# Performance work log

Measured on AMD Instinct MI355X. Metric: run time of the kernel, lower is better.

## Reference

```python
import jax, jax.numpy as jnp
import numpy as np

SEP = 64  # separate_number


def _get_histogram(M, sep):
    # torch code detaches + moves to CPU: no gradient flows through the histogram
    M = jax.lax.stop_gradient(M)
    mn = jnp.min(M)
    mx = jnp.max(M)
    interval = (mx - mn) / sep
    # equal-width binning; last bin is inclusive of max (clip handles it)
    idx = jnp.clip(jnp.floor((M - mn) / interval).astype(jnp.int32), 0, sep - 1)
    hist = jnp.zeros((sep,), dtype=M.dtype).at[idx.ravel()].add(1.0)
    return jax.nn.sigmoid(hist)


def setup_inputs() -> dict:
    key = jax.random.key(0)
    k1, k2, k3 = jax.random.split(key, 3)
    N, D = 8192, 256
    current_feature = jax.random.normal(k1, (N, D), dtype=jnp.float32)
    previous_feature = jax.random.normal(k2, (N, D), dtype=jnp.float32)
    # nn.Linear(separate_number, hidden_dim=1, bias=False) weight: [1, SEP]
    W = jax.random.normal(k3, (1, SEP), dtype=jnp.float32) * (1.0 / np.sqrt(SEP))
    return {"current_feature": current_feature, "previous_feature": previous_feature, "W": W}


def reference(current_feature, previous_feature, W):
    sep = W.shape[1]
    # [N, N] similarity matrix
    M = jnp.matmul(current_feature, previous_feature.T)
    hist_left = _get_histogram(M, sep)
    # result_matrix_right = prev @ cur.T = M.T; a transpose has an identical
    # value histogram, so reuse M (same math, avoids a second NxN matmul)
    hist_right = _get_histogram(M, sep)
    beta = (hist_left + hist_right) / 2.0
    beta = jnp.matmul(beta, W.T)  # Linear, no bias -> [hidden_dim]
    return jax.nn.sigmoid(beta)
```

## Files before the change

kernel.cpp:

```cpp
#include <hip/hip_runtime.h>

typedef __attribute__((ext_vector_type(8))) short short8v;
typedef __attribute__((ext_vector_type(4))) float f32x4;

#define N_ROWS 8192
#define KSPLIT 768
#define SEP 64
#define TDET 65.0f
#define TEXACT 73.0f
#define VTOL 5.5f
#define LIST_CAP 524288u

__device__ inline unsigned f2ord(float x){
  unsigned u = __float_as_uint(x);
  return (u & 0x80000000u) ? ~u : (u | 0x80000000u);
}
__device__ inline float ord2f(unsigned u){
  unsigned b = (u & 0x80000000u) ? (u & 0x7fffffffu) : ~u;
  return __uint_as_float(b);
}
__device__ inline unsigned short bf16rn(float x){
  unsigned b = __float_as_uint(x);
  unsigned r = (b + 0x7fffu + ((b >> 16) & 1u)) >> 16;
  return (unsigned short)r;
}
__device__ inline void gload16(const void* g, void* l){
  __builtin_amdgcn_global_load_lds((const __attribute__((address_space(1))) void*)g,
                                   (__attribute__((address_space(3))) void*)l, 16, 0, 0);
}
__device__ inline int bin_of(float v, float mnv, float interval){
  float r = (v - mnv) / interval;
  int b = (int)floorf(r);
  return b < 0 ? 0 : (b > 63 ? 63 : b);
}

__global__ void split_kernel(const float* __restrict__ cur, const float* __restrict__ prev,
                             unsigned short* __restrict__ cur2, unsigned short* __restrict__ prev2,
                             unsigned* __restrict__ ctl){
  if (blockIdx.x == 0){
    if (threadIdx.x == 0){
      ctl[0] = 0xFFFFFFFFu; ctl[1] = 0u; ctl[2] = 1u; ctl[3] = 0u; ctl[4] = 0u; ctl[5] = 0u;
    }
    if (threadIdx.x < 64) ctl[6 + threadIdx.x] = 0u;
  }
  int g = blockIdx.x * blockDim.x + threadIdx.x;
  int isB = (g >= (N_ROWS * 256 / 4)) ? 1 : 0;
  int t = g - isB * (N_ROWS * 256 / 4);
  const float4 v = ((const float4*)(isB ? prev : cur))[t];
  int row = t >> 6;
  int col = (t & 63) << 2;
  float xs[4] = {v.x, v.y, v.z, v.w};
  unsigned short h[4], l[4];
  #pragma unroll
  for (int j = 0; j < 4; ++j){
    unsigned short hb = bf16rn(xs[j]);
    float hf = __uint_as_float(((unsigned)hb) << 16);
    h[j] = hb;
    l[j] = bf16rn(xs[j] - hf);
  }
  unsigned short* dst = isB ? prev2 : cur2;
  size_t base = (size_t)row * KSPLIT + col;
  uint2 hw, lw;
  hw.x = (unsigned)h[0] | ((unsigned)h[1] << 16); hw.y = (unsigned)h[2] | ((unsigned)h[3] << 16);
  lw.x = (unsigned)l[0] | ((unsigned)l[1] << 16); lw.y = (unsigned)l[2] | ((unsigned)l[3] << 16);
  *(uint2*)(dst + base) = hw;
  if (!isB){
    *(uint2*)(dst + base + 256) = lw;
    *(uint2*)(dst + base + 512) = hw;
  } else {
    *(uint2*)(dst + base + 256) = hw;
    *(uint2*)(dst + base + 512) = lw;
  }
}

template<int EPI, int KSTEPS>
__global__ __launch_bounds__(256) void gemm_kernel(const unsigned short* __restrict__ A2,
                                                   const unsigned short* __restrict__ B2,
                                                   unsigned* __restrict__ mm,
                                                   unsigned* __restrict__ hist,
                                                   unsigned* __restrict__ idxq,
                                                   unsigned* __restrict__ lcnt,
                                                   const unsigned* __restrict__ flag){
  if (EPI == 0 || EPI == 2){
    if (flag[0] == 0u) return;
  }
  __shared__ unsigned short As[128 * 32];
  __shared__ unsigned short Bs[128 * 32];

  const int tid  = threadIdx.x;
  const int lane = tid & 63;
  const int wave = tid >> 6;
  const int swz = ((blockIdx.x & 7) << 9) | (blockIdx.x >> 3);
  const int bm = swz >> 6;
  const int bn = swz & 63;
  const int wr = wave >> 1, wc = wave & 1;

  const size_t aBase = (size_t)bm * 128 * KSPLIT;
  const size_t bBase = (size_t)bn * 128 * KSPLIT;
  const int id0 = tid, id1 = tid + 256;
  const size_t aOff0 = aBase + (size_t)(id0 >> 2) * KSPLIT + (id0 & 3) * 8;
  const size_t aOff1 = aBase + (size_t)(id1 >> 2) * KSPLIT + (id1 & 3) * 8;
  const size_t bOff0 = bBase + (size_t)(id0 >> 2) * KSPLIT + (id0 & 3) * 8;
  const size_t bOff1 = bBase + (size_t)(id1 >> 2) * KSPLIT + (id1 & 3) * 8;

  f32x4 acc[4][4];
  #pragma unroll
  for (int m = 0; m < 4; ++m)
    #pragma unroll
    for (int n = 0; n < 4; ++n)
      acc[m][n] = (f32x4){0.f, 0.f, 0.f, 0.f};

  const int rsel = lane & 15;
  const int ksel = (lane >> 4) * 8;

  for (int ks = 0; ks < KSTEPS; ++ks){
    const int k0 = ks * 32;
    gload16(A2 + aOff0 + k0, As + id0 * 8);
    gload16(A2 + aOff1 + k0, As + id1 * 8);
    gload16(B2 + bOff0 + k0, Bs + id0 * 8);
    gload16(B2 + bOff1 + k0, Bs + id1 * 8);
    __syncthreads();
    short8v a[4], b[4];
    #pragma unroll
    for (int m = 0; m < 4; ++m)
      a[m] = *(const short8v*)(As + (wr * 64 + m * 16 + rsel) * 32 + ksel);
    #pragma unroll
    for (int n = 0; n < 4; ++n)
      b[n] = *(const short8v*)(Bs + (wc * 64 + n * 16 + rsel) * 32 + ksel);
    #pragma unroll
    for (int m = 0; m < 4; ++m)
      #pragma unroll
      for (int n = 0; n < 4; ++n)
        acc[m][n] = __builtin_amdgcn_mfma_f32_16x16x32_bf16(a[m], b[n], acc[m][n], 0, 0, 0);
    __syncthreads();
  }

  float*    red = (float*)As;
  unsigned* lh  = (unsigned*)((char*)As + 64);

  if (EPI == 0){
    float mn = 3.4e38f, mx = -3.4e38f;
    #pragma unroll
    for (int m = 0; m < 4; ++m)
      #pragma unroll
      for (int n = 0; n < 4; ++n)
        #pragma unroll
        for (int q = 0; q < 4; ++q){
          float v = acc[m][n][q];
          mn = fminf(mn, v); mx = fmaxf(mx, v);
        }
    #pragma unroll
    for (int off = 32; off; off >>= 1){
      mn = fminf(mn, __shfl_xor(mn, off));
      mx = fmaxf(mx, __shfl_xor(mx, off));
    }
    if (lane == 0){ red[wave] = mn; red[4 + wave] = mx; }
    __syncthreads();
    if (tid == 0){
      mn = fminf(fminf(red[0], red[1]), fminf(red[2], red[3]));
      mx = fmaxf(fmaxf(red[4], red[5]), fmaxf(red[6], red[7]));
      atomicMin(mm + 0, f2ord(mn));
      atomicMax(mm + 1, f2ord(mx));
    }
  }
  if (EPI == 2){
    if (tid < SEP) lh[tid] = 0u;
    __syncthreads();
    const float mnv = ord2f(mm[0]);
    const float mxv = ord2f(mm[1]);
    const float interval = (mxv - mnv) / 64.0f;
    #pragma unroll
    for (int m = 0; m < 4; ++m)
      #pragma unroll
      for (int n = 0; n < 4; ++n)
        #pragma unroll
        for (int q = 0; q < 4; ++q)
          atomicAdd(&lh[bin_of(acc[m][n][q], mnv, interval)], 1u);
    __syncthreads();
    if (tid < SEP){ unsigned c = lh[tid]; if (c) atomicAdd(hist + tid, c); }
  }
  if (EPI == 4){
    unsigned long long mask = 0ull;
    #pragma unroll
    for (int m = 0; m < 4; ++m)
      #pragma unroll
      for (int n = 0; n < 4; ++n)
        #pragma unroll
        for (int q = 0; q < 4; ++q){
          int b = (m * 4 + n) * 4 + q;
          if (fabsf(acc[m][n][q]) > TDET) mask |= (1ull << b);
        }
    int cnt = __popcll(mask);
    int pre = cnt;
    #pragma unroll
    for (int off = 1; off < 64; off <<= 1){
      int t = __shfl_up(pre, off);
      if (lane >= off) pre += t;
    }
    int tot = __shfl(pre, 63);
    int base = 0;
    if (lane == 63 && tot > 0) base = (int)atomicAdd(lcnt, (unsigned)tot);
    base = __shfl(base, 63);
    if (mask){
      unsigned kk = (unsigned)(base + pre - cnt);
      #pragma unroll
      for (int m = 0; m < 4; ++m)
        #pragma unroll
        for (int n = 0; n < 4; ++n)
          #pragma unroll
          for (int q = 0; q < 4; ++q){
            int b = (m * 4 + n) * 4 + q;
            if ((mask >> b) & 1ull){
              float v = acc[m][n][q];
              int i = bm * 128 + wr * 64 + m * 16 + ((lane >> 4) << 2) + q;
              int j = bn * 128 + wc * 64 + n * 16 + (lane & 15);
              int e = (int)((v + 144.0f) * (1.0f / 4.5f));
              e = e < 0 ? 0 : (e > 63 ? 63 : e);
              if (kk < LIST_CAP)
                idxq[kk] = ((unsigned)e << 26) | ((unsigned)i << 13) | (unsigned)j;
              ++kk;
            }
          }
    }
  }
}

__global__ __launch_bounds__(256) void recompute_kernel(const float* __restrict__ cur,
                                                        const float* __restrict__ prev,
                                                        const unsigned* __restrict__ idxq,
                                                        const unsigned* __restrict__ lcnt,
                                                        unsigned* __restrict__ mm,
                                                        unsigned* __restrict__ viol,
                                                        float* __restrict__ vex,
                                                        const float* __restrict__ W,
                                                        unsigned* __restrict__ flag,
                                                        float* __restrict__ out,
                                                        unsigned* __restrict__ done){
  const int lane = threadIdx.x & 63;
  const int w  = (blockIdx.x * blockDim.x + threadIdx.x) >> 6;
  const int nw = (gridDim.x * blockDim.x) >> 6;
  unsigned n = lcnt[0]; if (n > LIST_CAP) n = LIST_CAP;
  float wmn = 3.4e38f, wmx = -3.4e38f;
  bool any = false;
  for (unsigned c = w; c < n; c += (unsigned)nw){
    unsigned u = idxq[c];
    int i = (int)((u >> 13) & 8191u), j = (int)(u & 8191u);
    float4 a = ((const float4*)cur)[i * 64 + lane];
    float4 b = ((const float4*)prev)[j * 64 + lane];
    float s = a.x * b.x + a.y * b.y + a.z * b.z + a.w * b.w;
    #pragma unroll
    for (int off = 32; off; off >>= 1) s += __shfl_xor(s, off);
    if (lane == 0){
      vex[c] = s;
      float dq = ((float)(u >> 26) + 0.5f) * 4.5f - 144.0f;
      if (fabsf(s - dq) > VTOL) atomicAdd(viol, 1u);
    }
    wmn = fminf(wmn, s); wmx = fmaxf(wmx, s);
    any = true;
  }
  if (lane == 0 && any){
    atomicMin(mm + 0, f2ord(wmn));
    atomicMax(mm + 1, f2ord(wmx));
  }

  __threadfence();
  __shared__ unsigned lastf;
  if (threadIdx.x == 0)
    lastf = (atomicAdd(done, 1u) == gridDim.x - 1u) ? 1u : 0u;
  __syncthreads();
  if (!lastf) return;
  __threadfence();

  __shared__ unsigned h[SEP];
  __shared__ unsigned okf;
  const int tid = threadIdx.x;
  if (tid < SEP) h[tid] = 0u;
  __syncthreads();
  const float mnv = ord2f(mm[0]);
  const float mxv = ord2f(mm[1]);
  const float interval = (mxv - mnv) / 64.0f;
  const unsigned cnt = lcnt[0];
  const unsigned n2 = cnt > LIST_CAP ? LIST_CAP : cnt;
  for (unsigned i2 = tid; i2 < n2; i2 += 256u)
    atomicAdd(&h[bin_of(vex[i2], mnv, interval)], 1u);
  __syncthreads();
  if (tid == 0){
    const int bLO = bin_of(-TEXACT, mnv, interval);
    const int bHI = bin_of( TEXACT, mnv, interval);
    bool ok = (cnt <= LIST_CAP) && (viol[0] == 0u) && (bLO >= 3) && (bHI <= 60) && (bLO < bHI)
              && (h[bLO - 1] >= 30u) && (h[bHI + 1] >= 30u);
    okf = ok ? 1u : 0u;
    if (ok) flag[0] = 0u;
  }
  __syncthreads();
  if (!okf) return;
  if (tid < 64){
    const int bLO = bin_of(-TEXACT, mnv, interval);
    const int bHI = bin_of( TEXACT, mnv, interval);
    float beta;
    if (tid < bLO || tid > bHI) beta = 1.f / (1.f + expf(-(float)h[tid]));
    else beta = 1.0f;
    float p = beta * W[tid];
    #pragma unroll
    for (int off = 32; off; off >>= 1) p += __shfl_down(p, off);
    if (tid == 0) out[0] = 1.f / (1.f + expf(-p));
  }
}

__global__ void fin_kernel(const unsigned* __restrict__ hist, const float* __restrict__ W,
                           const unsigned* __restrict__ flag, float* __restrict__ out){
  if (flag[0] == 0u) return;
  int j = threadIdx.x;
  float beta = 1.f / (1.f + expf(-(float)hist[j]));
  float p = beta * W[j];
  #pragma unroll
  for (int off = 32; off; off >>= 1) p += __shfl_down(p, off);
  if (j == 0) out[0] = 1.f / (1.f + expf(-p));
}

extern "C" void kernel_launch(void* const* d_in, const int* in_sizes, int n_in,
                              void* d_out, int out_size, void* d_ws, size_t ws_size,
                              hipStream_t stream){
  const float* cur  = (const float*)d_in[0];
  const float* prev = (const float*)d_in[1];
  const float* W    = (const float*)d_in[2];
  float* out = (float*)d_out;
  char* ws = (char*)d_ws;

  unsigned short* cur2  = (unsigned short*)ws;
  unsigned short* prev2 = (unsigned short*)(ws + 12582912);
  unsigned* ctl   = (unsigned*)(ws + 25165824);
  unsigned* mm    = ctl + 0;
  unsigned* flag  = ctl + 2;
  unsigned* lcnt  = ctl + 3;
  unsigned* viol  = ctl + 4;
  unsigned* done  = ctl + 5;
  unsigned* hist  = ctl + 6;
  unsigned* idxq  = (unsigned*)(ws + 25166592);
  float*    vex   = (float*)(ws + 27263744);
  const size_t NEED_NEW = 29360896;

  split_kernel<<<4096, 256, 0, stream>>>(cur, prev, cur2, prev2, ctl);

  if (ws_size >= NEED_NEW){
    gemm_kernel<4, 8><<<4096, 256, 0, stream>>>(cur2, prev2, mm, hist, idxq, lcnt, flag);
    recompute_kernel<<<256, 256, 0, stream>>>(cur, prev, idxq, lcnt, mm, viol, vex,
                                              W, flag, out, done);
    gemm_kernel<0, 24><<<4096, 256, 0, stream>>>(cur2, prev2, mm, hist, idxq, lcnt, flag);
    gemm_kernel<2, 24><<<4096, 256, 0, stream>>>(cur2, prev2, mm, hist, idxq, lcnt, flag);
    fin_kernel<<<1, 64, 0, stream>>>(hist, W, flag, out);
  } else {
    gemm_kernel<0, 24><<<4096, 256, 0, stream>>>(cur2, prev2, mm, hist, idxq, lcnt, flag);
    gemm_kernel<2, 24><<<4096, 256, 0, stream>>>(cur2, prev2, mm, hist, idxq, lcnt, flag);
    fin_kernel<<<1, 64, 0, stream>>>(hist, W, flag, out);
  }
}
```

Measured before the change: 188.5 us.

## Store hi/lo bf16 split once and fetch two K-chunks per barrier in detection GEMM

The split kernel now writes only the hi and lo bf16 planes (row stride 512 instead of 768), which cuts split-kernel writes and workspace size. The full GEMM indexes segments so it still computes the three-term hi*hi + lo*hi + hi*lo product. A dedicated detection GEMM loads two 32-wide K slices per synchronisation (double-size LDS) to halve the number of barriers. Doubling shared memory in the detection kernel may lower occupancy.

```diff
diff --git a/kernel.cpp b/kernel.cpp
--- a/kernel.cpp
+++ b/kernel.cpp
@@ -4,7 +4,7 @@
 typedef __attribute__((ext_vector_type(4))) float f32x4;
 
 #define N_ROWS 8192
-#define KSPLIT 768
+#define KS2 512
 #define SEP 64
 #define TDET 65.0f
 #define TEXACT 73.0f
@@ -59,33 +59,20 @@
     l[j] = bf16rn(xs[j] - hf);
   }
   unsigned short* dst = isB ? prev2 : cur2;
-  size_t base = (size_t)row * KSPLIT + col;
+  size_t base = (size_t)row * KS2 + col;
   uint2 hw, lw;
   hw.x = (unsigned)h[0] | ((unsigned)h[1] << 16); hw.y = (unsigned)h[2] | ((unsigned)h[3] << 16);
   lw.x = (unsigned)l[0] | ((unsigned)l[1] << 16); lw.y = (unsigned)l[2] | ((unsigned)l[3] << 16);
   *(uint2*)(dst + base) = hw;
-  if (!isB){
-    *(uint2*)(dst + base + 256) = lw;
-    *(uint2*)(dst + base + 512) = hw;
-  } else {
-    *(uint2*)(dst + base + 256) = hw;
-    *(uint2*)(dst + base + 512) = lw;
-  }
-}
-
-template<int EPI, int KSTEPS>
-__global__ __launch_bounds__(256) void gemm_kernel(const unsigned short* __restrict__ A2,
-                                                   const unsigned short* __restrict__ B2,
-                                                   unsigned* __restrict__ mm,
-                                                   unsigned* __restrict__ hist,
-                                                   unsigned* __restrict__ idxq,
-                                                   unsigned* __restrict__ lcnt,
-                                                   const unsigned* __restrict__ flag){
-  if (EPI == 0 || EPI == 2){
-    if (flag[0] == 0u) return;
-  }
-  __shared__ unsigned short As[128 * 32];
-  __shared__ unsigned short Bs[128 * 32];
+  *(uint2*)(dst + base + 256) = lw;
+}
+
+__global__ __launch_bounds__(256) void gemm_det(const unsigned short* __restrict__ A2,
+                                                const unsigned short* __restrict__ B2,
+                                                unsigned* __restrict__ idxq,
+                                                unsigned* __restrict__ lcnt){
+  __shared__ unsigned short As[2][128 * 32];
+  __shared__ unsigned short Bs[2][128 * 32];
 
   const int tid  = threadIdx.x;
   const int lane = tid & 63;
@@ -95,13 +82,13 @@
   const int bn = swz & 63;
   const int wr = wave >> 1, wc = wave & 1;
 
-  const size_t aBase = (size_t)bm * 128 * KSPLIT;
-  const size_t bBase = (size_t)bn * 128 * KSPLIT;
+  const size_t aBase = (size_t)bm * 128 * KS2;
+  const size_t bBase = (size_t)bn * 128 * KS2;
   const int id0 = tid, id1 = tid + 256;
-  const size_t aOff0 = aBase + (size_t)(id0 >> 2) * KSPLIT + (id0 & 3) * 8;
-  const size_t aOff1 = aBase + (size_t)(id1 >> 2) * KSPLIT + (id1 & 3) * 8;
-  const size_t bOff0 = bBase + (size_t)(id0 >> 2) * KSPLIT + (id0 & 3) * 8;
-  const size_t bOff1 = bBase + (size_t)(id1 >> 2) * KSPLIT + (id1 & 3) * 8;
+  const size_t aOff0 = aBase + (size_t)(id0 >> 2) * KS2 + (id0 & 3) * 8;
+  const size_t aOff1 = aBase + (size_t)(id1 >> 2) * KS2 + (id1 & 3) * 8;
+  const size_t bOff0 = bBase + (size_t)(id0 >> 2) * KS2 + (id0 & 3) * 8;
+  const size_t bOff1 = bBase + (size_t)(id1 >> 2) * KS2 + (id1 & 3) * 8;
 
   f32x4 acc[4][4];
   #pragma unroll
@@ -113,12 +100,124 @@
   const int rsel = lane & 15;
   const int ksel = (lane >> 4) * 8;
 
-  for (int ks = 0; ks < KSTEPS; ++ks){
-    const int k0 = ks * 32;
-    gload16(A2 + aOff0 + k0, As + id0 * 8);
-    gload16(A2 + aOff1 + k0, As + id1 * 8);
-    gload16(B2 + bOff0 + k0, Bs + id0 * 8);
-    gload16(B2 + bOff1 + k0, Bs + id1 * 8);
+  for (int st = 0; st < 4; ++st){
+    const int k0 = st * 64;
+    gload16(A2 + aOff0 + k0,      &As[0][id0 * 8]);
+    gload16(A2 + aOff1 + k0,      &As[0][id1 * 8]);
+    gload16(B2 + bOff0 + k0,      &Bs[0][id0 * 8]);
+    gload16(B2 + bOff1 + k0,      &Bs[0][id1 * 8]);
+    gload16(A2 + aOff0 + k0 + 32, &As[1][id0 * 8]);
+    gload16(A2 + aOff1 + k0 + 32, &As[1][id1 * 8]);
+    gload16(B2 + bOff0 + k0 + 32, &Bs[1][id0 * 8]);
+    gload16(B2 + bOff1 + k0 + 32, &Bs[1][id1 * 8]);
+    __syncthreads();
+    #pragma unroll
+    for (int p = 0; p < 2; ++p){
+      short8v a[4], b[4];
+      #pragma unroll
+      for (int m = 0; m < 4; ++m)
+        a[m] = *(const short8v*)(&As[p][(wr * 64 + m * 16 + rsel) * 32 + ksel]);
+      #pragma unroll
+      for (int n = 0; n < 4; ++n)
+        b[n] = *(const short8v*)(&Bs[p][(wc * 64 + n * 16 + rsel) * 32 + ksel]);
+      #pragma unroll
+      for (int m = 0; m < 4; ++m)
+        #pragma unroll
+        for (int n = 0; n < 4; ++n)
+          acc[m][n] = __builtin_amdgcn_mfma_f32_16x16x32_bf16(a[m], b[n], acc[m][n], 0, 0, 0);
+    }
+    __syncthreads();
+  }
+
+  unsigned long long mask = 0ull;
+  #pragma unroll
+  for (int m = 0; m < 4; ++m)
+    #pragma unroll
+    for (int n = 0; n < 4; ++n)
+      #pragma unroll
+      for (int q = 0; q < 4; ++q){
+        int b = (m * 4 + n) * 4 + q;
+        if (fabsf(acc[m][n][q]) > TDET) mask |= (1ull << b);
+      }
+  int cnt = __popcll(mask);
+  int pre = cnt;
+  #pragma unroll
+  for (int off = 1; off < 64; off <<= 1){
+    int t = __shfl_up(pre, off);
+    if (lane >= off) pre += t;
+  }
+  int tot = __shfl(pre, 63);
+  int base = 0;
+  if (lane == 63 && tot > 0) base = (int)atomicAdd(lcnt, (unsigned)tot);
+  base = __shfl(base, 63);
+  if (mask){
+    unsigned kk = (unsigned)(base + pre - cnt);
+    #pragma unroll
+    for (int m = 0; m < 4; ++m)
+      #pragma unroll
+      for (int n = 0; n < 4; ++n)
+        #pragma unroll
+        for (int q = 0; q < 4; ++q){
+          int b = (m * 4 + n) * 4 + q;
+          if ((mask >> b) & 1ull){
+            float v = acc[m][n][q];
+            int i = bm * 128 + wr * 64 + m * 16 + ((lane >> 4) << 2) + q;
+            int j = bn * 128 + wc * 64 + n * 16 + (lane & 15);
+            int e = (int)((v + 144.0f) * (1.0f / 4.5f));
+            e = e < 0 ? 0 : (e > 63 ? 63 : e);
+            if (kk < LIST_CAP)
+              idxq[kk] = ((unsigned)e << 26) | ((unsigned)i << 13) | (unsigned)j;
+            ++kk;
+          }
+        }
+  }
+}
+
+template<int EPI>
+__global__ __launch_bounds__(256) void gemm_kernel(const unsigned short* __restrict__ A2,
+                                                   const unsigned short* __restrict__ B2,
+                                                   unsigned* __restrict__ mm,
+                                                   unsigned* __restrict__ hist,
+                                                   const unsigned* __restrict__ flag){
+  if (flag[0] == 0u) return;
+  __shared__ unsigned short As[128 * 32];
+  __shared__ unsigned short Bs[128 * 32];
+
+  const int tid  = threadIdx.x;
+  const int lane = tid & 63;
+  const int wave = tid >> 6;
+  const int swz = ((blockIdx.x & 7) << 9) | (blockIdx.x >> 3);
+  const int bm = swz >> 6;
+  const int bn = swz & 63;
+  const int wr = wave >> 1, wc = wave & 1;
+
+  const size_t aBase = (size_t)bm * 128 * KS2;
+  const size_t bBase = (size_t)bn * 128 * KS2;
+  const int id0 = tid, id1 = tid + 256;
+  const size_t aOff0 = aBase + (size_t)(id0 >> 2) * KS2 + (id0 & 3) * 8;
+  const size_t aOff1 = aBase + (size_t)(id1 >> 2) * KS2 + (id1 & 3) * 8;
+  const size_t bOff0 = bBase + (size_t)(id0 >> 2) * KS2 + (id0 & 3) * 8;
+  const size_t bOff1 = bBase + (size_t)(id1 >> 2) * KS2 + (id1 & 3) * 8;
+
+  f32x4 acc[4][4];
+  #pragma unroll
+  for (int m = 0; m < 4; ++m)
+    #pragma unroll
+    for (int n = 0; n < 4; ++n)
+      acc[m][n] = (f32x4){0.f, 0.f, 0.f, 0.f};
+
+  const int rsel = lane & 15;
+  const int ksel = (lane >> 4) * 8;
+
+  for (int ks = 0; ks < 24; ++ks){
+    const int seg = ks >> 3;
+    const int kk  = (ks & 7) * 32;
+    const int aK0 = (seg == 1) ? 256 + kk : kk;
+    const int bK0 = (seg == 2) ? 256 + kk : kk;
+    gload16(A2 + aOff0 + aK0, As + id0 * 8);
+    gload16(A2 + aOff1 + aK0, As + id1 * 8);
+    gload16(B2 + bOff0 + bK0, Bs + id0 * 8);
+    gload16(B2 + bOff1 + bK0, Bs + id1 * 8);
     __syncthreads();
     short8v a[4], b[4];
     #pragma unroll
@@ -178,50 +277,6 @@
           atomicAdd(&lh[bin_of(acc[m][n][q], mnv, interval)], 1u);
     __syncthreads();
     if (tid < SEP){ unsigned c = lh[tid]; if (c) atomicAdd(hist + tid, c); }
-  }
-  if (EPI == 4){
-    unsigned long long mask = 0ull;
-    #pragma unroll
-    for (int m = 0; m < 4; ++m)
-      #pragma unroll
-      for (int n = 0; n < 4; ++n)
-        #pragma unroll
-        for (int q = 0; q < 4; ++q){
-          int b = (m * 4 + n) * 4 + q;
-          if (fabsf(acc[m][n][q]) > TDET) mask |= (1ull << b);
-        }
-    int cnt = __popcll(mask);
-    int pre = cnt;
-    #pragma unroll
-    for (int off = 1; off < 64; off <<= 1){
-      int t = __shfl_up(pre, off);
-      if (lane >= off) pre += t;
-    }
-    int tot = __shfl(pre, 63);
-    int base = 0;
-    if (lane == 63 && tot > 0) base = (int)atomicAdd(lcnt, (unsigned)tot);
-    base = __shfl(base, 63);
-    if (mask){
-      unsigned kk = (unsigned)(base + pre - cnt);
-      #pragma unroll
-      for (int m = 0; m < 4; ++m)
-        #pragma unroll
-        for (int n = 0; n < 4; ++n)
-          #pragma unroll
-          for (int q = 0; q < 4; ++q){
-            int b = (m * 4 + n) * 4 + q;
-            if ((mask >> b) & 1ull){
-              float v = acc[m][n][q];
-              int i = bm * 128 + wr * 64 + m * 16 + ((lane >> 4) << 2) + q;
-              int j = bn * 128 + wc * 64 + n * 16 + (lane & 15);
-              int e = (int)((v + 144.0f) * (1.0f / 4.5f));
-              e = e < 0 ? 0 : (e > 63 ? 63 : e);
-              if (kk < LIST_CAP)
-                idxq[kk] = ((unsigned)e << 26) | ((unsigned)i << 13) | (unsigned)j;
-              ++kk;
-            }
-          }
-    }
   }
 }
 
@@ -328,30 +383,30 @@
   char* ws = (char*)d_ws;
 
   unsigned short* cur2  = (unsigned short*)ws;
-  unsigned short* prev2 = (unsigned short*)(ws + 12582912);
-  unsigned* ctl   = (unsigned*)(ws + 25165824);
+  unsigned short* prev2 = (unsigned short*)(ws + 8388608);
+  unsigned* ctl   = (unsigned*)(ws + 16777216);
   unsigned* mm    = ctl + 0;
   unsigned* flag  = ctl + 2;
   unsigned* lcnt  = ctl + 3;
   unsigned* viol  = ctl + 4;
   unsigned* done  = ctl + 5;
   unsigned* hist  = ctl + 6;
-  unsigned* idxq  = (unsigned*)(ws + 25166592);
-  float*    vex   = (float*)(ws + 27263744);
-  const size_t NEED_NEW = 29360896;
+  unsigned* idxq  = (unsigned*)(ws + 16777728);
+  float*    vex   = (float*)(ws + 18874880);
+  const size_t NEED_NEW = 20972032;
 
   split_kernel<<<4096, 256, 0, stream>>>(cur, prev, cur2, prev2, ctl);
 
   if (ws_size >= NEED_NEW){
-    gemm_kernel<4, 8><<<4096, 256, 0, stream>>>(cur2, prev2, mm, hist, idxq, lcnt, flag);
+    gemm_det<<<4096, 256, 0, stream>>>(cur2, prev2, idxq, lcnt);
     recompute_kernel<<<256, 256, 0, stream>>>(cur, prev, idxq, lcnt, mm, viol, vex,
                                               W, flag, out, done);
-    gemm_kernel<0, 24><<<4096, 256, 0, stream>>>(cur2, prev2, mm, hist, idxq, lcnt, flag);
-    gemm_kernel<2, 24><<<4096, 256, 0, stream>>>(cur2, prev2, mm, hist, idxq, lcnt, flag);
+    gemm_kernel<0><<<4096, 256, 0, stream>>>(cur2, prev2, mm, hist, flag);
+    gemm_kernel<2><<<4096, 256, 0, stream>>>(cur2, prev2, mm, hist, flag);
     fin_kernel<<<1, 64, 0, stream>>>(hist, W, flag, out);
   } else {
-    gemm_kernel<0, 24><<<4096, 256, 0, stream>>>(cur2, prev2, mm, hist, idxq, lcnt, flag);
-    gemm_kernel<2, 24><<<4096, 256, 0, stream>>>(cur2, prev2, mm, hist, idxq, lcnt, flag);
+    gemm_kernel<0><<<4096, 256, 0, stream>>>(cur2, prev2, mm, hist, flag);
+    gemm_kernel<2><<<4096, 256, 0, stream>>>(cur2, prev2, mm, hist, flag);
     fin_kernel<<<1, 64, 0, stream>>>(hist, W, flag, out);
   }
 }
```

New measurement: 182.1 us. -3.4%, faster.
